# Kernel tuning notes

Hardware: AMD Instinct MI355X
Metric: run time of the kernel (lower is better)

Reference implementation:

```python
import jax, jax.numpy as jnp
import numpy as np

B_G = 16        # number of point clouds
N_PER = 32768   # points per cloud (equal -> no padding)
T = B_G * N_PER
CIN = 16
D = 32          # global_dim
H = 4           # num_heads
HD = D // H
L = 2           # layers
EPS_LN = 1e-5
EPS_Z = 1e-6


def setup_inputs() -> dict:
    key = jax.random.key(0)
    ks = jax.random.split(key, 32)
    r = lambda i, shape, s: (jax.random.normal(ks[i], shape, dtype=jnp.float32) * s)
    inp = {
        "x": r(0, (T, CIN), 1.0),
        "pos": r(1, (T, 3), 1.0),
        "batch": (jnp.arange(T, dtype=jnp.int32) // N_PER),
        "w_in": r(2, (CIN, D), CIN ** -0.5),
        "b_in": r(3, (D,), 0.02),
        "w_pos": r(4, (3, D), 3 ** -0.5),
        "b_pos": r(5, (D,), 0.02),
        "wq": r(6, (L, D, D), D ** -0.5),
        "bq": r(7, (L, D), 0.02),
        "wk": r(8, (L, D, D), D ** -0.5),
        "bk": r(9, (L, D), 0.02),
        "wv": r(10, (L, D, D), D ** -0.5),
        "bv": r(11, (L, D), 0.02),
        "wo": r(12, (L, D, D), D ** -0.5),
        "bo": r(13, (L, D), 0.02),
        "g1": jnp.ones((L, D), jnp.float32),
        "be1": jnp.zeros((L, D), jnp.float32),
        "w1": r(14, (L, D, 2 * D), D ** -0.5),
        "bf1": r(15, (L, 2 * D), 0.02),
        "w2": r(16, (L, 2 * D, D), (2 * D) ** -0.5),
        "bf2": r(17, (L, D), 0.02),
        "g2": jnp.ones((L, D), jnp.float32),
        "be2": jnp.zeros((L, D), jnp.float32),
    }
    return inp


def _layernorm(h, g, b):
    mu = jnp.mean(h, axis=-1, keepdims=True)
    var = jnp.mean(jnp.square(h - mu), axis=-1, keepdims=True)
    return (h - mu) * jax.lax.rsqrt(var + EPS_LN) * g + b


def _linear_attn(h, wq, bq, wk, bk, wv, bv, wo, bo):
    B, N, C = h.shape
    def heads(w, b):
        return (h @ w + b).reshape(B, N, H, HD).transpose(0, 2, 1, 3)  # [B,H,N,hd]
    q = jax.nn.elu(heads(wq, bq)) + 1.0   # ELU feature map phi(.)
    k = jax.nn.elu(heads(wk, bk)) + 1.0
    v = heads(wv, bv)
    kv = jnp.einsum("bhnd,bhne->bhde", k, v)            # O(N) KV summary
    ksum = k.sum(axis=2)                                   # [B,H,hd]
    z = 1.0 / (jnp.einsum("bhnd,bhd->bhn", q, ksum) + EPS_Z)
    out = jnp.einsum("bhnd,bhde->bhne", q, kv) * z[..., None]
    out = out.transpose(0, 2, 1, 3).reshape(B, N, C)
    return out @ wo + bo


def reference(x, pos, batch, w_in, b_in, w_pos, b_pos, wq, bq, wk, bk, wv, bv,
              wo, bo, g1, be1, w1, bf1, w2, bf2, g2, be2):
    # to_dense_batch: batch is sorted; compute per-point index within its segment
    counts = jax.ops.segment_sum(jnp.ones((T,), jnp.int32), batch, num_segments=B_G)
    starts = jnp.concatenate([jnp.zeros((1,), jnp.int32), jnp.cumsum(counts)[:-1]])
    idx = jnp.arange(T, dtype=jnp.int32) - starts[batch]
    x_dense = jnp.zeros((B_G, N_PER, CIN), x.dtype).at[batch, idx].set(x)
    pos_dense = jnp.zeros((B_G, N_PER, 3), pos.dtype).at[batch, idx].set(pos)

    h = (x_dense @ w_in + b_in) + (pos_dense @ w_pos + b_pos)  # [B,N,D]
    for l in range(L):
        h = _layernorm(h + _linear_attn(h, wq[l], bq[l], wk[l], bk[l],
                                        wv[l], bv[l], wo[l], bo[l]), g1[l], be1[l])
        ffn = jax.nn.relu(h @ w1[l] + bf1[l]) @ w2[l] + bf2[l]
        h = _layernorm(h + ffn, g2[l], be2[l])
    return h[batch, idx]  # back to [T, D] (h[mask])
```

## Files before the change

### kernel.cpp

```cpp
#include <hip/hip_runtime.h>

#define KVSZ 288
#define EPS_LN 1e-5f
#define EPS_Z  1e-6f

typedef __attribute__((ext_vector_type(8))) short bf16x8;
typedef __attribute__((ext_vector_type(4))) float f32x4;

#define MFMA(a, b, c) __builtin_amdgcn_mfma_f32_16x16x32_bf16(a, b, c, 0, 0, 0)

#define PWE 0
#define LBASE(l) (1024 + (l) * 8192)
#define PQ 0
#define PO 1024
#define P1 2048
#define P2 4096
#define PK 6144
#define PV 7168

__device__ __forceinline__ unsigned short f2bf(float f) {
  union { float f; unsigned u; } x; x.f = f;
  unsigned r = x.u + 0x7fff + ((x.u >> 16) & 1);
  return (unsigned short)(r >> 16);
}

__device__ __forceinline__ unsigned pkbf(float a, float b) {
#if __has_builtin(__builtin_amdgcn_cvt_pk_bf16_f32)
  typedef __attribute__((ext_vector_type(2))) __bf16 bf16x2_t;
  bf16x2_t v = __builtin_amdgcn_cvt_pk_bf16_f32(a, b);
  return __builtin_bit_cast(unsigned, v);
#else
  return (unsigned)f2bf(a) | ((unsigned)f2bf(b) << 16);
#endif
}

__device__ __forceinline__ float bfu(unsigned short s) {
  union { float f; unsigned u; } x; x.u = ((unsigned)s) << 16; return x.f;
}

__device__ __forceinline__ void lds_fence() { asm volatile("s_waitcnt lgkmcnt(0)" ::: "memory"); }
__device__ __forceinline__ float phi(float x) { return x > 0.f ? x + 1.f : __expf(x); }

__device__ __forceinline__ int perm32(int kp) {
  return ((kp & 4) << 2) | (((kp >> 3) << 2) + (kp & 3));
}

__device__ __forceinline__ bf16x8 bbuild(f32x4 lo, f32x4 hi) {
  union { bf16x8 v; unsigned u[4]; } cv;
  cv.u[0] = pkbf(lo[0], lo[1]); cv.u[1] = pkbf(lo[2], lo[3]);
  cv.u[2] = pkbf(hi[0], hi[1]); cv.u[3] = pkbf(hi[2], hi[3]);
  return cv.v;
}

__device__ __forceinline__ void stage_a32(unsigned short* dst, const float* __restrict__ W,
                                          int N, int tid) {
  for (int i = tid; i < 32 * N; i += 256) {
    int n = i >> 5, kp = i & 31;
    dst[i] = f2bf(W[perm32(kp) * N + n]);
  }
}
__device__ __forceinline__ void stage_a64(unsigned short* dst, const float* __restrict__ W,
                                          int tid) {
  for (int i = tid; i < 64 * 32; i += 256) {
    int n = i >> 6, kp = i & 63;
    int kl = ((kp >> 5) << 5) + perm32(kp & 31);
    dst[i] = f2bf(W[kl * 32 + n]);
  }
}

__device__ __forceinline__ void stage_kvm_lds(unsigned short* dst,
                                              const float* __restrict__ kvg, int tid) {
  for (int i = tid; i < 1024; i += 256) {
    int e = i >> 5, kp = i & 31;
    int d = perm32(kp);
    float v = ((d >> 3) == (e >> 3)) ? kvg[(e >> 3) * 64 + (d & 7) * 8 + (e & 7)] : 0.f;
    dst[i] = f2bf(v);
  }
}

__device__ __forceinline__ void ln_t(f32x4& a0, f32x4& a1, float4 g0, float4 g1,
                                     float4 b0, float4 b1) {
  float s = a0[0] + a0[1] + a0[2] + a0[3] + a1[0] + a1[1] + a1[2] + a1[3];
  s += __shfl_xor(s, 16); s += __shfl_xor(s, 32);
  float mu = s * (1.f / 32.f);
  float vv = 0.f;
#pragma unroll
  for (int r = 0; r < 4; r++) {
    a0[r] -= mu; a1[r] -= mu;
    vv += a0[r] * a0[r] + a1[r] * a1[r];
  }
  vv += __shfl_xor(vv, 16); vv += __shfl_xor(vv, 32);
  float rstd = rsqrtf(vv * (1.f / 32.f) + EPS_LN);
  a0[0] = a0[0] * rstd * g0.x + b0.x; a0[1] = a0[1] * rstd * g0.y + b0.y;
  a0[2] = a0[2] * rstd * g0.z + b0.z; a0[3] = a0[3] * rstd * g0.w + b0.w;
  a1[0] = a1[0] * rstd * g1.x + b1.x; a1[1] = a1[1] * rstd * g1.y + b1.y;
  a1[2] = a1[2] * rstd * g1.z + b1.z; a1[3] = a1[3] * rstd * g1.w + b1.w;
}

__device__ __forceinline__ void layer_core_l(
    f32x4 (&hc0)[4], f32x4 (&hc1)[4], const bf16x8 (&hBp)[4],
    const unsigned short* lw, const unsigned short* kvm, const float* kss,
    int quad, int m,
    const float* __restrict__ bq, const float* __restrict__ bo,
    const float* __restrict__ g1, const float* __restrict__ be1,
    const float* __restrict__ bf1, const float* __restrict__ bf2,
    const float* __restrict__ g2, const float* __restrict__ be2) {
  const int k0 = quad * 8, q4 = quad * 4;
  {
    const bf16x8 wqA0 = *(const bf16x8*)(lw + PQ + m * 32 + k0);
    const bf16x8 wqA1 = *(const bf16x8*)(lw + PQ + (16 + m) * 32 + k0);
    const bf16x8 woA0 = *(const bf16x8*)(lw + PO + m * 32 + k0);
    const bf16x8 woA1 = *(const bf16x8*)(lw + PO + (16 + m) * 32 + k0);
    const bf16x8 kvA0 = *(const bf16x8*)(kvm + m * 32 + k0);
    const bf16x8 kvA1 = *(const bf16x8*)(kvm + (16 + m) * 32 + k0);
    const float4 bq0 = *(const float4*)(bq + q4), bq1 = *(const float4*)(bq + 16 + q4);
    const float4 bo0 = *(const float4*)(bo + q4), bo1 = *(const float4*)(bo + 16 + q4);
    const float4 g10 = *(const float4*)(g1 + q4), g11 = *(const float4*)(g1 + 16 + q4);
    const float4 e10 = *(const float4*)(be1 + q4), e11 = *(const float4*)(be1 + 16 + q4);
    const float4 ks0 = *(const float4*)(kss + q4);
    const float4 ks1 = *(const float4*)(kss + 16 + q4);
#pragma unroll
    for (int mt = 0; mt < 4; mt++) {
      f32x4 q0 = {bq0.x, bq0.y, bq0.z, bq0.w};
      f32x4 q1 = {bq1.x, bq1.y, bq1.z, bq1.w};
      q0 = MFMA(wqA0, hBp[mt], q0);
      q1 = MFMA(wqA1, hBp[mt], q1);
#pragma unroll
      for (int r = 0; r < 4; r++) { q0[r] = phi(q0[r]); q1[r] = phi(q1[r]); }
      bf16x8 qB = bbuild(q0, q1);
      f32x4 zz = {0.f, 0.f, 0.f, 0.f};
      f32x4 at0 = MFMA(kvA0, qB, zz);
      f32x4 at1 = MFMA(kvA1, qB, zz);
      float p0 = q0[0] * ks0.x + q0[1] * ks0.y + q0[2] * ks0.z + q0[3] * ks0.w;
      float p1 = q1[0] * ks1.x + q1[1] * ks1.y + q1[2] * ks1.z + q1[3] * ks1.w;
      p0 += __shfl_xor(p0, 16);
      p1 += __shfl_xor(p1, 16);
      float z0 = 1.f / (p0 + EPS_Z), z1 = 1.f / (p1 + EPS_Z);
      bf16x8 aB;
      {
        union { bf16x8 v; unsigned u[4]; } cv;
        cv.u[0] = pkbf(at0[0] * z0, at0[1] * z0); cv.u[1] = pkbf(at0[2] * z0, at0[3] * z0);
        cv.u[2] = pkbf(at1[0] * z1, at1[1] * z1); cv.u[3] = pkbf(at1[2] * z1, at1[3] * z1);
        aB = cv.v;
      }
      f32x4 h0 = hc0[mt], h1 = hc1[mt];
      h0[0] += bo0.x; h0[1] += bo0.y; h0[2] += bo0.z; h0[3] += bo0.w;
      h1[0] += bo1.x; h1[1] += bo1.y; h1[2] += bo1.z; h1[3] += bo1.w;
      h0 = MFMA(woA0, aB, h0);
      h1 = MFMA(woA1, aB, h1);
      ln_t(h0, h1, g10, g11, e10, e11);
      hc0[mt] = h0; hc1[mt] = h1;
    }
  }
  {
    bf16x8 w1A[4]; float4 b1f[4];
#pragma unroll
    for (int nt = 0; nt < 4; nt++) {
      w1A[nt] = *(const bf16x8*)(lw + P1 + (nt * 16 + m) * 32 + k0);
      b1f[nt] = *(const float4*)(bf1 + nt * 16 + q4);
    }
    const bf16x8 w2L0 = *(const bf16x8*)(lw + P2 + m * 64 + k0);
    const bf16x8 w2H0 = *(const bf16x8*)(lw + P2 + m * 64 + 32 + k0);
    const bf16x8 w2L1 = *(const bf16x8*)(lw + P2 + (16 + m) * 64 + k0);
    const bf16x8 w2H1 = *(const bf16x8*)(lw + P2 + (16 + m) * 64 + 32 + k0);
    const float4 b20 = *(const float4*)(bf2 + q4), b21 = *(const float4*)(bf2 + 16 + q4);
    const float4 g20 = *(const float4*)(g2 + q4), g21 = *(const float4*)(g2 + 16 + q4);
    const float4 e20 = *(const float4*)(be2 + q4), e21 = *(const float4*)(be2 + 16 + q4);
#pragma unroll
    for (int mt = 0; mt < 4; mt++) {
      bf16x8 hB = bbuild(hc0[mt], hc1[mt]);
      f32x4 hd[4];
#pragma unroll
      for (int nt = 0; nt < 4; nt++) {
        f32x4 ini = {b1f[nt].x, b1f[nt].y, b1f[nt].z, b1f[nt].w};
        hd[nt] = MFMA(w1A[nt], hB, ini);
#pragma unroll
        for (int r = 0; r < 4; r++) hd[nt][r] = fmaxf(hd[nt][r], 0.f);
      }
      bf16x8 fL = bbuild(hd[0], hd[1]);
      bf16x8 fH = bbuild(hd[2], hd[3]);
      f32x4 o0 = hc0[mt], o1 = hc1[mt];
      o0[0] += b20.x; o0[1] += b20.y; o0[2] += b20.z; o0[3] += b20.w;
      o1[0] += b21.x; o1[1] += b21.y; o1[2] += b21.z; o1[3] += b21.w;
      o0 = MFMA(w2L0, fL, o0);
      o0 = MFMA(w2H0, fH, o0);
      o1 = MFMA(w2L1, fL, o1);
      o1 = MFMA(w2H1, fH, o1);
      ln_t(o0, o1, g20, g21, e20, e21);
      hc0[mt] = o0; hc1[mt] = o1;
    }
  }
}

__device__ __forceinline__ void kv_stage_l(
    const bf16x8 (&hBp)[4], unsigned short* tw,
    const unsigned short* lwK, const unsigned short* lwV,
    float* blk, int quad, int m,
    const float* __restrict__ bk, const float* __restrict__ bv) {
  const int k0 = quad * 8, q4 = quad * 4;
  unsigned short* Tk = tw;
  unsigned short* Tv = tw + 1280;
  const bf16x8 wkA0 = *(const bf16x8*)(lwK + m * 32 + k0);
  const bf16x8 wkA1 = *(const bf16x8*)(lwK + (16 + m) * 32 + k0);
  const bf16x8 wvA0 = *(const bf16x8*)(lwV + m * 32 + k0);
  const bf16x8 wvA1 = *(const bf16x8*)(lwV + (16 + m) * 32 + k0);
  const float4 bk0 = *(const float4*)(bk + q4), bk1 = *(const float4*)(bk + 16 + q4);
  const float4 bv0 = *(const float4*)(bv + q4), bv1 = *(const float4*)(bv + 16 + q4);
  f32x4 accA = {0.f, 0.f, 0.f, 0.f}, accB = {0.f, 0.f, 0.f, 0.f};
  f32x4 ksa0 = {0.f, 0.f, 0.f, 0.f}, ksa1 = {0.f, 0.f, 0.f, 0.f};
#pragma unroll
  for (int ch = 0; ch < 2; ch++) {
#pragma unroll
    for (int mtl = 0; mtl < 2; mtl++) {
      int mt = ch * 2 + mtl;
      f32x4 kn0 = {bk0.x, bk0.y, bk0.z, bk0.w};
      f32x4 kn1 = {bk1.x, bk1.y, bk1.z, bk1.w};
      f32x4 vn0 = {bv0.x, bv0.y, bv0.z, bv0.w};
      f32x4 vn1 = {bv1.x, bv1.y, bv1.z, bv1.w};
      kn0 = MFMA(wkA0, hBp[mt], kn0);
      kn1 = MFMA(wkA1, hBp[mt], kn1);
      vn0 = MFMA(wvA0, hBp[mt], vn0);
      vn1 = MFMA(wvA1, hBp[mt], vn1);
      int cb = mtl * 16 + m;
#pragma unroll
      for (int r = 0; r < 4; r++) {
        kn0[r] = phi(kn0[r]); kn1[r] = phi(kn1[r]);
        ksa0[r] += kn0[r];    ksa1[r] += kn1[r];
        Tk[(q4 + r) * 40 + cb]      = f2bf(kn0[r]);
        Tk[(16 + q4 + r) * 40 + cb] = f2bf(kn1[r]);
        Tv[(q4 + r) * 40 + cb]      = f2bf(vn0[r]);
        Tv[(16 + q4 + r) * 40 + cb] = f2bf(vn1[r]);
      }
    }
    lds_fence();
    bf16x8 akL = *(const bf16x8*)(Tk + m * 40 + k0);
    bf16x8 akH = *(const bf16x8*)(Tk + (16 + m) * 40 + k0);
    bf16x8 avL = *(const bf16x8*)(Tv + m * 40 + k0);
    bf16x8 avH = *(const bf16x8*)(Tv + (16 + m) * 40 + k0);
    accA = MFMA(akL, avL, accA);
    accB = MFMA(akH, avH, accB);
    lds_fence();
  }
#pragma unroll
  for (int r = 0; r < 4; r++) {
    float v0 = ksa0[r], v1 = ksa1[r];
    v0 += __shfl_xor(v0, 1); v0 += __shfl_xor(v0, 2); v0 += __shfl_xor(v0, 4); v0 += __shfl_xor(v0, 8);
    v1 += __shfl_xor(v1, 1); v1 += __shfl_xor(v1, 2); v1 += __shfl_xor(v1, 4); v1 += __shfl_xor(v1, 8);
    if (m == 0) {
      atomicAdd(&blk[256 + q4 + r], v0);
      atomicAdd(&blk[272 + q4 + r], v1);
    }
  }
  if ((quad >> 1) == (m >> 3)) {
    int h0 = quad >> 1, h1 = 2 + (quad >> 1), e = m & 7;
#pragma unroll
    for (int r = 0; r < 4; r++) {
      int d = (q4 + r) & 7;
      atomicAdd(&blk[h0 * 64 + d * 8 + e], accA[r]);
      atomicAdd(&blk[h1 * 64 + d * 8 + e], accB[r]);
    }
  }
}

__global__ __launch_bounds__(256) void k_prep(
    const float* __restrict__ w_in, const float* __restrict__ w_pos,
    const float* __restrict__ wq, const float* __restrict__ wk,
    const float* __restrict__ wv, const float* __restrict__ wo,
    const float* __restrict__ w1, const float* __restrict__ w2,
    unsigned short* __restrict__ pw) {
  const int tid = threadIdx.x;
  for (int i = tid; i < 1024; i += 256) {
    int n = i >> 5, k = i & 31;
    float v = k < 16 ? w_in[k * 32 + n] : (k < 19 ? w_pos[(k - 16) * 32 + n] : 0.f);
    pw[PWE + i] = f2bf(v);
  }
  for (int l = 0; l < 2; l++) {
    unsigned short* b = pw + LBASE(l);
    stage_a32(b + PQ, wq + l * 1024, 32, tid);
    stage_a32(b + PO, wo + l * 1024, 32, tid);
    stage_a32(b + P1, w1 + l * 2048, 64, tid);
    stage_a64(b + P2, w2 + l * 2048, tid);
    stage_a32(b + PK, wk + l * 1024, 32, tid);
    stage_a32(b + PV, wv + l * 1024, 32, tid);
  }
}

template <int H16>
__global__ __launch_bounds__(256) void k_embed(
    const float* __restrict__ x, const float* __restrict__ pos,
    const float* __restrict__ b_in, const float* __restrict__ b_pos,
    const float* __restrict__ bk, const float* __restrict__ bv,
    const unsigned short* __restrict__ pw, unsigned short* __restrict__ hb,
    float* __restrict__ hf, float* __restrict__ gkv) {
  __shared__ __align__(16) unsigned short lws[3072];
  __shared__ __align__(16) unsigned short tiles[4 * 2560];
  __shared__ float blk[KVSZ];
  const int tid = threadIdx.x;
  const int wv_ = tid >> 6, lane = tid & 63, quad = lane >> 4, m = lane & 15;
  unsigned short* tw = tiles + wv_ * 2560;
  const int cloud = blockIdx.x >> 7;
  const int wbase = blockIdx.x * 256 + wv_ * 64;
  const int k0 = quad * 8, q4 = quad * 4;
  for (int j = tid; j < 384; j += 256) {
    int i = j * 8;
    const unsigned short* src = (i < 1024) ? (pw + PWE + i)
                                           : (pw + LBASE(0) + PK + (i - 1024));
    *(bf16x8*)(lws + i) = *(const bf16x8*)src;
  }
  for (int i = tid; i < KVSZ; i += 256) blk[i] = 0.f;
  __syncthreads();
  const bf16x8 weA0 = *(const bf16x8*)(lws + m * 32 + k0);
  const bf16x8 weA1 = *(const bf16x8*)(lws + (16 + m) * 32 + k0);
  float4 bi0, bi1;
  {
    float4 a = *(const float4*)(b_in + q4), b = *(const float4*)(b_pos + q4);
    bi0 = make_float4(a.x + b.x, a.y + b.y, a.z + b.z, a.w + b.w);
    float4 c = *(const float4*)(b_in + 16 + q4), d = *(const float4*)(b_pos + 16 + q4);
    bi1 = make_float4(c.x + d.x, c.y + d.y, c.z + d.z, c.w + d.w);
  }
  bf16x8 fr[4];
#pragma unroll
  for (int mt = 0; mt < 4; mt++) {
    int p = wbase + mt * 16 + m;
    union { bf16x8 v; unsigned u[4]; } xb;
    xb.u[0] = xb.u[1] = xb.u[2] = xb.u[3] = 0;
    if (quad < 2) {
      const float4* xp = (const float4*)(x + (size_t)p * 16 + quad * 8);
      float4 t0 = xp[0], t1 = xp[1];
      xb.u[0] = pkbf(t0.x, t0.y); xb.u[1] = pkbf(t0.z, t0.w);
      xb.u[2] = pkbf(t1.x, t1.y); xb.u[3] = pkbf(t1.z, t1.w);
    } else if (quad == 2) {
      const float* pp = pos + (size_t)p * 3;
      xb.u[0] = pkbf(pp[0], pp[1]); xb.u[1] = pkbf(pp[2], 0.f);
    }
    f32x4 i0 = {bi0.x, bi0.y, bi0.z, bi0.w};
    f32x4 i1 = {bi1.x, bi1.y, bi1.z, bi1.w};
    f32x4 h0 = MFMA(weA0, xb.v, i0);
    f32x4 h1 = MFMA(weA1, xb.v, i1);
    fr[mt] = bbuild(h0, h1);
    if (H16) {
      *(bf16x8*)(hb + ((size_t)p * 32 + quad * 8)) = fr[mt];
    } else {
      float* hp = hf + (size_t)p * 32;
      *(float4*)(hp + q4)      = make_float4(h0[0], h0[1], h0[2], h0[3]);
      *(float4*)(hp + 16 + q4) = make_float4(h1[0], h1[1], h1[2], h1[3]);
    }
  }
  kv_stage_l(fr, tw, lws + 1024, lws + 2048, blk, quad, m, bk, bv);
  __syncthreads();
  float* g = gkv + cloud * KVSZ;
  for (int i = tid; i < KVSZ; i += 256) atomicAdd(&g[i], blk[i]);
}

template <int H16>
__global__ __launch_bounds__(256) void k_mid(
    const float* __restrict__ bq, const float* __restrict__ bo,
    const float* __restrict__ g1, const float* __restrict__ be1,
    const float* __restrict__ bf1, const float* __restrict__ bf2,
    const float* __restrict__ g2, const float* __restrict__ be2,
    const float* __restrict__ bkn, const float* __restrict__ bvn,
    const unsigned short* __restrict__ pw, const float* __restrict__ kv_in,
    float* __restrict__ gkv_out, unsigned short* __restrict__ hb,
    float* __restrict__ hf) {
  __shared__ __align__(16) unsigned short lws[8192];
  __shared__ __align__(16) unsigned short kvm[1024];
  __shared__ __align__(16) float kss[32];
  __shared__ __align__(16) unsigned short tiles[4 * 2560];
  __shared__ float blk[KVSZ];
  const int tid = threadIdx.x;
  const int wv_ = tid >> 6, lane = tid & 63, quad = lane >> 4, m = lane & 15;
  unsigned short* tw = tiles + wv_ * 2560;
  const int cloud = blockIdx.x >> 7;
  const int wbase = blockIdx.x * 256 + wv_ * 64;
  const int q4 = quad * 4;
  const float* kvg = kv_in + cloud * KVSZ;
  for (int j = tid; j < 1024; j += 256) {
    int i = j * 8;
    const unsigned short* src = (i < 6144) ? (pw + LBASE(0) + i)
                                           : (pw + LBASE(1) + PK + (i - 6144));
    *(bf16x8*)(lws + i) = *(const bf16x8*)src;
  }
  stage_kvm_lds(kvm, kvg, tid);
  if (tid < 32) kss[tid] = kvg[256 + tid];
  for (int i = tid; i < KVSZ; i += 256) blk[i] = 0.f;
  __syncthreads();
  f32x4 hc0[4], hc1[4];
  bf16x8 fr[4];
#pragma unroll
  for (int mt = 0; mt < 4; mt++) {
    int p = wbase + mt * 16 + m;
    if (H16) {
      fr[mt] = *(const bf16x8*)(hb + ((size_t)p * 32 + quad * 8));
#pragma unroll
      for (int r = 0; r < 4; r++) {
        hc0[mt][r] = bfu((unsigned short)fr[mt][r]);
        hc1[mt][r] = bfu((unsigned short)fr[mt][4 + r]);
      }
    } else {
      const float* hp = hf + (size_t)p * 32;
      float4 lo = *(const float4*)(hp + q4);
      float4 hi = *(const float4*)(hp + 16 + q4);
      hc0[mt][0] = lo.x; hc0[mt][1] = lo.y; hc0[mt][2] = lo.z; hc0[mt][3] = lo.w;
      hc1[mt][0] = hi.x; hc1[mt][1] = hi.y; hc1[mt][2] = hi.z; hc1[mt][3] = hi.w;
      fr[mt] = bbuild(hc0[mt], hc1[mt]);
    }
  }
  layer_core_l(hc0, hc1, fr, lws, kvm, kss, quad, m,
               bq, bo, g1, be1, bf1, bf2, g2, be2);
#pragma unroll
  for (int mt = 0; mt < 4; mt++) {
    int p = wbase + mt * 16 + m;
    fr[mt] = bbuild(hc0[mt], hc1[mt]);
    if (H16) {
      *(bf16x8*)(hb + ((size_t)p * 32 + quad * 8)) = fr[mt];
    } else {
      float* hp = hf + (size_t)p * 32;
      *(float4*)(hp + q4)      = make_float4(hc0[mt][0], hc0[mt][1], hc0[mt][2], hc0[mt][3]);
      *(float4*)(hp + 16 + q4) = make_float4(hc1[mt][0], hc1[mt][1], hc1[mt][2], hc1[mt][3]);
    }
  }
  kv_stage_l(fr, tw, lws + 6144, lws + 7168, blk, quad, m, bkn, bvn);
  __syncthreads();
  float* g = gkv_out + cloud * KVSZ;
  for (int i = tid; i < KVSZ; i += 256) atomicAdd(&g[i], blk[i]);
}

template <int H16>
__global__ __launch_bounds__(256) void k_last(
    const float* __restrict__ bq, const float* __restrict__ bo,
    const float* __restrict__ g1, const float* __restrict__ be1,
    const float* __restrict__ bf1, const float* __restrict__ bf2,
    const float* __restrict__ g2, const float* __restrict__ be2,
    const unsigned short* __restrict__ pw, const float* __restrict__ kv_in,
    const unsigned short* __restrict__ hb, float* __restrict__ out) {
  __shared__ __align__(16) unsigned short lws[6144];
  __shared__ __align__(16) unsigned short kvm[1024];
  __shared__ __align__(16) float kss[32];
  const int tid = threadIdx.x;
  const int wv_ = tid >> 6, lane = tid & 63, quad = lane >> 4, m = lane & 15;
  const int cloud = blockIdx.x >> 7;
  const int wbase = blockIdx.x * 256 + wv_ * 64;
  const int q4 = quad * 4;
  const float* kvg = kv_in + cloud * KVSZ;
  for (int j = tid; j < 768; j += 256)
    *(bf16x8*)(lws + j * 8) = *(const bf16x8*)(pw + LBASE(1) + j * 8);
  stage_kvm_lds(kvm, kvg, tid);
  if (tid < 32) kss[tid] = kvg[256 + tid];
  __syncthreads();
  f32x4 hc0[4], hc1[4];
  bf16x8 fr[4];
#pragma unroll
  for (int mt = 0; mt < 4; mt++) {
    int p = wbase + mt * 16 + m;
    if (H16) {
      fr[mt] = *(const bf16x8*)(hb + ((size_t)p * 32 + quad * 8));
#pragma unroll
      for (int r = 0; r < 4; r++) {
        hc0[mt][r] = bfu((unsigned short)fr[mt][r]);
        hc1[mt][r] = bfu((unsigned short)fr[mt][4 + r]);
      }
    } else {
      const float* hp = out + (size_t)p * 32;
      float4 lo = *(const float4*)(hp + q4);
      float4 hi = *(const float4*)(hp + 16 + q4);
      hc0[mt][0] = lo.x; hc0[mt][1] = lo.y; hc0[mt][2] = lo.z; hc0[mt][3] = lo.w;
      hc1[mt][0] = hi.x; hc1[mt][1] = hi.y; hc1[mt][2] = hi.z; hc1[mt][3] = hi.w;
      fr[mt] = bbuild(hc0[mt], hc1[mt]);
    }
  }
  layer_core_l(hc0, hc1, fr, lws, kvm, kss, quad, m,
               bq, bo, g1, be1, bf1, bf2, g2, be2);
#pragma unroll
  for (int mt = 0; mt < 4; mt++) {
    int p = wbase + mt * 16 + m;
    float* hp = out + (size_t)p * 32;
    *(float4*)(hp + q4)      = make_float4(hc0[mt][0], hc0[mt][1], hc0[mt][2], hc0[mt][3]);
    *(float4*)(hp + 16 + q4) = make_float4(hc1[mt][0], hc1[mt][1], hc1[mt][2], hc1[mt][3]);
  }
}

extern "C" void kernel_launch(void* const* d_in, const int* in_sizes, int n_in,
                              void* d_out, int out_size, void* d_ws, size_t ws_size,
                              hipStream_t stream) {
  (void)in_sizes; (void)n_in; (void)out_size;
  const float* x     = (const float*)d_in[0];
  const float* pos   = (const float*)d_in[1];
  const float* w_in  = (const float*)d_in[3];
  const float* b_in  = (const float*)d_in[4];
  const float* w_pos = (const float*)d_in[5];
  const float* b_pos = (const float*)d_in[6];
  const float* wq  = (const float*)d_in[7];
  const float* bq  = (const float*)d_in[8];
  const float* wk  = (const float*)d_in[9];
  const float* bk  = (const float*)d_in[10];
  const float* wv  = (const float*)d_in[11];
  const float* bv  = (const float*)d_in[12];
  const float* wo  = (const float*)d_in[13];
  const float* bo  = (const float*)d_in[14];
  const float* g1  = (const float*)d_in[15];
  const float* be1 = (const float*)d_in[16];
  const float* w1  = (const float*)d_in[17];
  const float* bf1 = (const float*)d_in[18];
  const float* w2  = (const float*)d_in[19];
  const float* bf2 = (const float*)d_in[20];
  const float* g2  = (const float*)d_in[21];
  const float* be2 = (const float*)d_in[22];
  float* out = (float*)d_out;
  float* kvbuf = (float*)d_ws;
  unsigned short* pw = (unsigned short*)((char*)d_ws + 40960);
  unsigned short* hb = (unsigned short*)((char*)d_ws + 131072);
  const size_t need = 131072ull + 524288ull * 32ull * 2ull;
  const bool h16 = ws_size >= need;

  hipMemsetAsync(kvbuf, 0, 2 * 16 * KVSZ * sizeof(float), stream);
  k_prep<<<dim3(1), dim3(256), 0, stream>>>(w_in, w_pos, wq, wk, wv, wo, w1, w2, pw);
  dim3 grid(2048), block(256);
  if (h16) {
    k_embed<1><<<grid, block, 0, stream>>>(x, pos, b_in, b_pos, bk, bv, pw, hb, out, kvbuf);
    k_mid<1><<<grid, block, 0, stream>>>(bq, bo, g1, be1, bf1, bf2, g2, be2,
                                         bk + 32, bv + 32, pw, kvbuf,
                                         kvbuf + 16 * KVSZ, hb, out);
    k_last<1><<<grid, block, 0, stream>>>(bq + 32, bo + 32, g1 + 32, be1 + 32,
                                          bf1 + 64, bf2 + 32, g2 + 32, be2 + 32,
                                          pw, kvbuf + 16 * KVSZ, hb, out);
  } else {
    k_embed<0><<<grid, block, 0, stream>>>(x, pos, b_in, b_pos, bk, bv, pw, hb, out, kvbuf);
    k_mid<0><<<grid, block, 0, stream>>>(bq, bo, g1, be1, bf1, bf2, g2, be2,
                                         bk + 32, bv + 32, pw, kvbuf,
                                         kvbuf + 16 * KVSZ, hb, out);
    k_last<0><<<grid, block, 0, stream>>>(bq + 32, bo + 32, g1 + 32, be1 + 32,
                                          bf1 + 64, bf2 + 32, g2 + 32, be2 + 32,
                                          pw, kvbuf + 16 * KVSZ, hb, out);
  }
}
```

Before: 256.8 us.

## Fold kv zeroing into multi-block prep and hoist global loads before LDS staging

The separate memset is removed: the KV accumulator is now zeroed inside the prep kernel, which runs on 64 blocks with a grid-stride loop instead of a single block. In the embed, mid and last kernels, the per-point input loads (x/pos or bf16 activations) are issued before weight staging and the barrier, so their latency overlaps the LDS fill. The aim is to cut launch count and serial prep time and to hide global-load latency, at the cost of more live registers across the staging phase.

```diff
diff --git a/kernel.cpp b/kernel.cpp
--- a/kernel.cpp
+++ b/kernel.cpp
@@ -53,15 +53,15 @@
 }
 
 __device__ __forceinline__ void stage_a32(unsigned short* dst, const float* __restrict__ W,
-                                          int N, int tid) {
-  for (int i = tid; i < 32 * N; i += 256) {
+                                          int N, int gt, int gs) {
+  for (int i = gt; i < 32 * N; i += gs) {
     int n = i >> 5, kp = i & 31;
     dst[i] = f2bf(W[perm32(kp) * N + n]);
   }
 }
 __device__ __forceinline__ void stage_a64(unsigned short* dst, const float* __restrict__ W,
-                                          int tid) {
-  for (int i = tid; i < 64 * 32; i += 256) {
+                                          int gt, int gs) {
+  for (int i = gt; i < 64 * 32; i += gs) {
     int n = i >> 6, kp = i & 63;
     int kl = ((kp >> 5) << 5) + perm32(kp & 31);
     dst[i] = f2bf(W[kl * 32 + n]);
@@ -267,21 +267,23 @@
     const float* __restrict__ wq, const float* __restrict__ wk,
     const float* __restrict__ wv, const float* __restrict__ wo,
     const float* __restrict__ w1, const float* __restrict__ w2,
-    unsigned short* __restrict__ pw) {
-  const int tid = threadIdx.x;
-  for (int i = tid; i < 1024; i += 256) {
+    unsigned short* __restrict__ pw, float* __restrict__ kvbuf) {
+  const int gt = blockIdx.x * 256 + threadIdx.x;
+  const int gs = gridDim.x * 256;
+  for (int i = gt; i < 2 * 16 * KVSZ; i += gs) kvbuf[i] = 0.f;
+  for (int i = gt; i < 1024; i += gs) {
     int n = i >> 5, k = i & 31;
     float v = k < 16 ? w_in[k * 32 + n] : (k < 19 ? w_pos[(k - 16) * 32 + n] : 0.f);
     pw[PWE + i] = f2bf(v);
   }
   for (int l = 0; l < 2; l++) {
     unsigned short* b = pw + LBASE(l);
-    stage_a32(b + PQ, wq + l * 1024, 32, tid);
-    stage_a32(b + PO, wo + l * 1024, 32, tid);
-    stage_a32(b + P1, w1 + l * 2048, 64, tid);
-    stage_a64(b + P2, w2 + l * 2048, tid);
-    stage_a32(b + PK, wk + l * 1024, 32, tid);
-    stage_a32(b + PV, wv + l * 1024, 32, tid);
+    stage_a32(b + PQ, wq + l * 1024, 32, gt, gs);
+    stage_a32(b + PO, wo + l * 1024, 32, gt, gs);
+    stage_a32(b + P1, w1 + l * 2048, 64, gt, gs);
+    stage_a64(b + P2, w2 + l * 2048, gt, gs);
+    stage_a32(b + PK, wk + l * 1024, 32, gt, gs);
+    stage_a32(b + PV, wv + l * 1024, 32, gt, gs);
   }
 }
 
@@ -301,6 +303,19 @@
   const int cloud = blockIdx.x >> 7;
   const int wbase = blockIdx.x * 256 + wv_ * 64;
   const int k0 = quad * 8, q4 = quad * 4;
+  float4 xt0[4], xt1[4];
+  float pp0[4], pp1[4], pp2[4];
+#pragma unroll
+  for (int mt = 0; mt < 4; mt++) {
+    int p = wbase + mt * 16 + m;
+    if (quad < 2) {
+      const float4* xp = (const float4*)(x + (size_t)p * 16 + quad * 8);
+      xt0[mt] = xp[0]; xt1[mt] = xp[1];
+    } else if (quad == 2) {
+      const float* pq = pos + (size_t)p * 3;
+      pp0[mt] = pq[0]; pp1[mt] = pq[1]; pp2[mt] = pq[2];
+    }
+  }
   for (int j = tid; j < 384; j += 256) {
     int i = j * 8;
     const unsigned short* src = (i < 1024) ? (pw + PWE + i)
@@ -325,13 +340,10 @@
     union { bf16x8 v; unsigned u[4]; } xb;
     xb.u[0] = xb.u[1] = xb.u[2] = xb.u[3] = 0;
     if (quad < 2) {
-      const float4* xp = (const float4*)(x + (size_t)p * 16 + quad * 8);
-      float4 t0 = xp[0], t1 = xp[1];
-      xb.u[0] = pkbf(t0.x, t0.y); xb.u[1] = pkbf(t0.z, t0.w);
-      xb.u[2] = pkbf(t1.x, t1.y); xb.u[3] = pkbf(t1.z, t1.w);
+      xb.u[0] = pkbf(xt0[mt].x, xt0[mt].y); xb.u[1] = pkbf(xt0[mt].z, xt0[mt].w);
+      xb.u[2] = pkbf(xt1[mt].x, xt1[mt].y); xb.u[3] = pkbf(xt1[mt].z, xt1[mt].w);
     } else if (quad == 2) {
-      const float* pp = pos + (size_t)p * 3;
-      xb.u[0] = pkbf(pp[0], pp[1]); xb.u[1] = pkbf(pp[2], 0.f);
+      xb.u[0] = pkbf(pp0[mt], pp1[mt]); xb.u[1] = pkbf(pp2[mt], 0.f);
     }
     f32x4 i0 = {bi0.x, bi0.y, bi0.z, bi0.w};
     f32x4 i1 = {bi1.x, bi1.y, bi1.z, bi1.w};
@@ -374,6 +386,14 @@
   const int wbase = blockIdx.x * 256 + wv_ * 64;
   const int q4 = quad * 4;
   const float* kvg = kv_in + cloud * KVSZ;
+  bf16x8 fr[4];
+  if (H16) {
+#pragma unroll
+    for (int mt = 0; mt < 4; mt++) {
+      int p = wbase + mt * 16 + m;
+      fr[mt] = *(const bf16x8*)(hb + ((size_t)p * 32 + quad * 8));
+    }
+  }
   for (int j = tid; j < 1024; j += 256) {
     int i = j * 8;
     const unsigned short* src = (i < 6144) ? (pw + LBASE(0) + i)
@@ -385,18 +405,16 @@
   for (int i = tid; i < KVSZ; i += 256) blk[i] = 0.f;
   __syncthreads();
   f32x4 hc0[4], hc1[4];
-  bf16x8 fr[4];
 #pragma unroll
   for (int mt = 0; mt < 4; mt++) {
-    int p = wbase + mt * 16 + m;
     if (H16) {
-      fr[mt] = *(const bf16x8*)(hb + ((size_t)p * 32 + quad * 8));
 #pragma unroll
       for (int r = 0; r < 4; r++) {
         hc0[mt][r] = bfu((unsigned short)fr[mt][r]);
         hc1[mt][r] = bfu((unsigned short)fr[mt][4 + r]);
       }
     } else {
+      int p = wbase + mt * 16 + m;
       const float* hp = hf + (size_t)p * 32;
       float4 lo = *(const float4*)(hp + q4);
       float4 hi = *(const float4*)(hp + 16 + q4);
@@ -442,24 +460,30 @@
   const int wbase = blockIdx.x * 256 + wv_ * 64;
   const int q4 = quad * 4;
   const float* kvg = kv_in + cloud * KVSZ;
+  bf16x8 fr[4];
+  if (H16) {
+#pragma unroll
+    for (int mt = 0; mt < 4; mt++) {
+      int p = wbase + mt * 16 + m;
+      fr[mt] = *(const bf16x8*)(hb + ((size_t)p * 32 + quad * 8));
+    }
+  }
   for (int j = tid; j < 768; j += 256)
     *(bf16x8*)(lws + j * 8) = *(const bf16x8*)(pw + LBASE(1) + j * 8);
   stage_kvm_lds(kvm, kvg, tid);
   if (tid < 32) kss[tid] = kvg[256 + tid];
   __syncthreads();
   f32x4 hc0[4], hc1[4];
-  bf16x8 fr[4];
 #pragma unroll
   for (int mt = 0; mt < 4; mt++) {
-    int p = wbase + mt * 16 + m;
     if (H16) {
-      fr[mt] = *(const bf16x8*)(hb + ((size_t)p * 32 + quad * 8));
 #pragma unroll
       for (int r = 0; r < 4; r++) {
         hc0[mt][r] = bfu((unsigned short)fr[mt][r]);
         hc1[mt][r] = bfu((unsigned short)fr[mt][4 + r]);
       }
     } else {
+      int p = wbase + mt * 16 + m;
       const float* hp = out + (size_t)p * 32;
       float4 lo = *(const float4*)(hp + q4);
       float4 hi = *(const float4*)(hp + 16 + q4);
@@ -512,8 +536,8 @@
   const size_t need = 131072ull + 524288ull * 32ull * 2ull;
   const bool h16 = ws_size >= need;
 
-  hipMemsetAsync(kvbuf, 0, 2 * 16 * KVSZ * sizeof(float), stream);
-  k_prep<<<dim3(1), dim3(256), 0, stream>>>(w_in, w_pos, wq, wk, wv, wo, w1, w2, pw);
+  k_prep<<<dim3(64), dim3(256), 0, stream>>>(w_in, w_pos, wq, wk, wv, wo, w1, w2,
+                                             pw, kvbuf);
   dim3 grid(2048), block(256);
   if (h16) {
     k_embed<1><<<grid, block, 0, stream>>>(x, pos, b_in, b_pos, bk, bv, pw, hb, out, kvbuf);
```

New measurement: 250.4 us. 2.5% less time.
